# Kernel tuning notes

Hardware: AMD Instinct MI355X
Metric: run time of the kernel (lower is better)

Reference implementation:

```python
import jax, jax.numpy as jnp
import numpy as np

KH = KW = 3
K = KH * KW
PAD = 1


def conv3x3(x, w, b):
    # x: [B,C,H,W], w: [O,C,3,3], b: [O]
    y = jax.lax.conv_general_dilated(x, w, (1, 1), ((PAD, PAD), (PAD, PAD)),
                                     dimension_numbers=('NCHW', 'OIHW', 'NCHW'))
    return y + b[None, :, None, None]


def deform_conv(x, offsets, w, b):
    # torchvision DeformConv2d, stride=1, pad=1, dilation=1, groups=1, offset_groups=1
    # x: [B,C,H,W], offsets: [B,2*K,H,W] ordered (dy,dx) per kernel point, w: [O,C,3,3]
    B, C, H, W = x.shape
    O = w.shape[0]
    off = offsets.reshape(B, K, 2, H, W)
    dy, dx = off[:, :, 0], off[:, :, 1]                      # [B,K,H,W]
    kyy, kxx = jnp.meshgrid(jnp.arange(KH), jnp.arange(KW), indexing='ij')
    ky = kyy.reshape(K).astype(x.dtype)
    kx = kxx.reshape(K).astype(x.dtype)
    py = dy + ky[None, :, None, None] + jnp.arange(H, dtype=x.dtype)[None, None, :, None] - PAD
    px = dx + kx[None, :, None, None] + jnp.arange(W, dtype=x.dtype)[None, None, None, :] - PAD
    y0 = jnp.floor(py)
    x0 = jnp.floor(px)
    wy = (py - y0)[:, None]                                   # [B,1,K,H,W]
    wx = (px - x0)[:, None]
    y0i = y0.astype(jnp.int32)
    x0i = x0.astype(jnp.int32)
    xf = x.reshape(B, C, H * W)

    def gather(yi, xi):
        valid = (yi >= 0) & (yi < H) & (xi >= 0) & (xi < W)   # zero outside
        yc = jnp.clip(yi, 0, H - 1)
        xc = jnp.clip(xi, 0, W - 1)
        idx = (yc * W + xc).reshape(B, 1, K * H * W)
        g = jnp.take_along_axis(xf, idx, axis=2).reshape(B, C, K, H, W)
        return g * valid[:, None].astype(x.dtype)

    v00 = gather(y0i, x0i)
    v01 = gather(y0i, x0i + 1)
    v10 = gather(y0i + 1, x0i)
    v11 = gather(y0i + 1, x0i + 1)
    samp = (v00 * (1 - wy) * (1 - wx) + v01 * (1 - wy) * wx
            + v10 * wy * (1 - wx) + v11 * wy * wx)            # [B,C,K,H,W]
    out = jnp.einsum('bckhw,ock->bohw', samp, w.reshape(O, C, K))
    return out + b[None, :, None, None]


def deform_align(x, y, wo, bo, wd, bd):
    return deform_conv(x, conv3x3(y, wo, bo), wd, bd)


def setup_inputs() -> dict:
    key = jax.random.key(0)
    ks = jax.random.split(key, 16)
    inC, embedC = 64, 96
    B, H, W = 4, 96, 96
    s = 0.02
    d = {
        'x1': jax.random.normal(ks[0], (B, inC, H, W), jnp.float32),
        'y': jax.random.normal(ks[1], (B, inC, H, W), jnp.float32),
        # block 1: offset conv inC->2K, deform conv inC->embedC
        'wo1': jax.random.normal(ks[2], (2 * K, inC, 3, 3), jnp.float32) * s,
        'bo1': jnp.zeros((2 * K,), jnp.float32),
        'wd1': jax.random.normal(ks[3], (embedC, inC, 3, 3), jnp.float32) * s,
        'bd1': jnp.zeros((embedC,), jnp.float32),
        # block 2: embedC->2K, embedC->embedC
        'wo2': jax.random.normal(ks[4], (2 * K, embedC, 3, 3), jnp.float32) * s,
        'bo2': jnp.zeros((2 * K,), jnp.float32),
        'wd2': jax.random.normal(ks[5], (embedC, embedC, 3, 3), jnp.float32) * s,
        'bd2': jnp.zeros((embedC,), jnp.float32),
        # block 3: embedC->2K, embedC->inC
        'wo3': jax.random.normal(ks[6], (2 * K, embedC, 3, 3), jnp.float32) * s,
        'bo3': jnp.zeros((2 * K,), jnp.float32),
        'wd3': jax.random.normal(ks[7], (inC, embedC, 3, 3), jnp.float32) * s,
        'bd3': jnp.zeros((inC,), jnp.float32),
    }
    return d


def reference(x1, y, wo1, bo1, wd1, bd1, wo2, bo2, wd2, bd2, wo3, bo3, wd3, bd3):
    h = deform_align(x1, y, wo1, bo1, wd1, bd1)
    h = deform_align(h, h, wo2, bo2, wd2, bd2)
    h = deform_align(h, h, wo3, bo3, wd3, bd3)
    return h
```

## Files before the change

### kernel.cpp

```cpp
#include <hip/hip_runtime.h>

constexpr int B = 4, H = 96, W = 96, HW = H * W;
constexpr int NPIX = B * HW;
constexpr int KOFF = 18;

typedef _Float16 half8 __attribute__((ext_vector_type(8)));
typedef _Float16 half4 __attribute__((ext_vector_type(4)));
typedef float f32x4 __attribute__((ext_vector_type(4)));

__device__ __forceinline__ int iclamp(int v, int lo, int hi) {
  return v < lo ? lo : (v > hi ? hi : v);
}

struct Corners {
  int i00, i01, i10, i11;
  float w00, w01, w10, w11;
};

__device__ __forceinline__ Corners mk_corners(float py, float qx) {
  float fy = floorf(py), fx = floorf(qx);
  float wy = py - fy, wx = qx - fx;
  int y0 = (int)fy, x0 = (int)fx;
  int y1 = y0 + 1, x1 = x0 + 1;
  bool vy0 = (y0 >= 0) & (y0 < H);
  bool vy1 = (y1 >= 0) & (y1 < H);
  bool vx0 = (x0 >= 0) & (x0 < W);
  bool vx1 = (x1 >= 0) & (x1 < W);
  int r0 = iclamp(y0, 0, H - 1) * W;
  int r1 = iclamp(y1, 0, H - 1) * W;
  int c0 = iclamp(x0, 0, W - 1);
  int c1 = iclamp(x1, 0, W - 1);
  Corners cc;
  cc.i00 = r0 + c0; cc.i01 = r0 + c1; cc.i10 = r1 + c0; cc.i11 = r1 + c1;
  float a = 1.f - wy, bb = 1.f - wx;
  cc.w00 = a * bb * ((vy0 & vx0) ? 1.f : 0.f);
  cc.w01 = a * wx * ((vy0 & vx1) ? 1.f : 0.f);
  cc.w10 = wy * bb * ((vy1 & vx0) ? 1.f : 0.f);
  cc.w11 = wy * wx * ((vy1 & vx1) ? 1.f : 0.f);
  return cc;
}

template <int KS>
__device__ __forceinline__ void load_corners(const _Float16* xb, int ch, const Corners& cc,
                                             half8 r[KS][4]) {
  const _Float16* p00 = xb + (size_t)cc.i00 * (KS * 32) + ch;
  const _Float16* p01 = xb + (size_t)cc.i01 * (KS * 32) + ch;
  const _Float16* p10 = xb + (size_t)cc.i10 * (KS * 32) + ch;
  const _Float16* p11 = xb + (size_t)cc.i11 * (KS * 32) + ch;
#pragma unroll
  for (int ks = 0; ks < KS; ++ks) {
    r[ks][0] = *(const half8*)(p00 + ks * 32);
    r[ks][1] = *(const half8*)(p01 + ks * 32);
    r[ks][2] = *(const half8*)(p10 + ks * 32);
    r[ks][3] = *(const half8*)(p11 + ks * 32);
  }
}

template <int KS>
__device__ __forceinline__ void interp_corners(const Corners& cc, half8 r[KS][4],
                                               half8 a[KS]) {
  _Float16 q00 = (_Float16)cc.w00, q01 = (_Float16)cc.w01;
  _Float16 q10 = (_Float16)cc.w10, q11 = (_Float16)cc.w11;
#pragma unroll
  for (int ks = 0; ks < KS; ++ks)
    a[ks] = r[ks][0] * q00 + r[ks][1] * q01 + r[ks][2] * q10 + r[ks][3] * q11;
}

template <int KS>
__device__ __forceinline__ void load_shift(const _Float16* xb, int ch, int h, int w,
                                           int ky, int kx, half8 a[KS]) {
  int yy = h + ky, xx = w + kx;
  bool v = (yy >= 0) & (yy < H) & (xx >= 0) & (xx < W);
  const _Float16* pv = xb + (size_t)(yy * W + xx) * (KS * 32) + ch;
#pragma unroll
  for (int ks = 0; ks < KS; ++ks) {
    half8 r = {0, 0, 0, 0, 0, 0, 0, 0};
    if (v) r = *(const half8*)(pv + ks * 32);
    a[ks] = r;
  }
}

template <int KS, int NJ>
__device__ __forceinline__ void mfma_tap1(const _Float16* wk, int lane,
                                          half8 a[KS], f32x4 acc[NJ]) {
#pragma unroll
  for (int ks = 0; ks < KS; ++ks)
#pragma unroll
    for (int j = 0; j < NJ; ++j) {
      half8 b = *(const half8*)(wk + ((size_t)(ks * NJ + j) * 64 + lane) * 8);
      acc[j] = __builtin_amdgcn_mfma_f32_16x16x32_f16(a[ks], b, acc[j], 0, 0, 0);
    }
}

struct WAll {
  const float* src[6];
  _Float16* dst[6];
  int C[6], Osrc[6], OPAD[6], base[6];
};

__global__ void wfrag_all_kernel(WAll wa) {
  int bid = blockIdx.x;
  int s = 0;
#pragma unroll
  for (int i = 1; i < 6; ++i) s += (bid >= wa.base[i]) ? 1 : 0;
  int fid = bid - wa.base[s];
  int C = wa.C[s], Osrc = wa.Osrc[s], OPAD = wa.OPAD[s];
  const float* wsrc = wa.src[s];
  _Float16* wf = wa.dst[s];
  int KS = C / 32;
  int NJ = OPAD / 16;
  int lane = threadIdx.x;
  int j = fid % NJ;
  int ks = (fid / NJ) % KS;
  int k = fid / (NJ * KS);
  int o = j * 16 + (lane & 15);
  int c0 = ks * 32 + (lane >> 4) * 8;
  half8 v;
#pragma unroll
  for (int u = 0; u < 8; ++u)
    v[u] = (o < Osrc) ? (_Float16)wsrc[((size_t)o * C + c0 + u) * 9 + k] : (_Float16)0.f;
  *(half8*)(wf + ((size_t)fid * 64 + lane) * 8) = v;
}

__global__ __launch_bounds__(256) void repack2_kernel(const float* __restrict__ in0,
                                                      const float* __restrict__ in1,
                                                      _Float16* __restrict__ o0,
                                                      _Float16* __restrict__ o1) {
  constexpr int C = 64;
  const float* in = blockIdx.y ? in1 : in0;
  _Float16* outh = blockIdx.y ? o1 : o0;
  __shared__ float tile[64 * C];
  int t = threadIdx.x;
  int pix0 = blockIdx.x * 64;
  int b = pix0 / HW;
  int hw0 = pix0 - b * HW;
  int l = t & 63;
  for (int cc = t >> 6; cc < C; cc += 4)
    tile[cc * 64 + l] = in[((size_t)b * C + cc) * HW + hw0 + l];
  __syncthreads();
  int pl = t >> 2;
  int cq = t & 3;
  _Float16* op = outh + (size_t)(pix0 + pl) * C + cq * (C / 4);
#pragma unroll
  for (int c = 0; c < C / 4; c += 4) {
    half4 hv;
#pragma unroll
    for (int u = 0; u < 4; ++u) hv[u] = (_Float16)tile[(cq * (C / 4) + c + u) * 64 + pl];
    *(half4*)(op + c) = hv;
  }
}

template <int C, int O, bool WF32, bool WH>
__global__ __launch_bounds__(64, 2)
void stage_kernel(const _Float16* __restrict__ xoff, const _Float16* __restrict__ xdef,
                  const _Float16* __restrict__ wfo, const float* __restrict__ bo,
                  const _Float16* __restrict__ wfd, const float* __restrict__ bd,
                  float* __restrict__ out, _Float16* __restrict__ outh) {
  constexpr int KS = C / 32;
  constexpr int NJ = O / 16;
  const int lane = threadIdx.x;
  const int row = lane & 15;
  const int kgrp = lane >> 4;
  const int ch = kgrp * 8;
  const int chunk = (blockIdx.x & 7) * (int)(gridDim.x >> 3) + (blockIdx.x >> 3);
  const int px0 = chunk * 16;
  const int b = px0 / HW;
  const int hw0 = px0 - b * HW;
  const int hwm = hw0 + row;
  const int h0 = hwm / W, w0 = hwm - h0 * W;
  const _Float16* xo = xoff + (size_t)b * HW * C;
  const _Float16* xd = xdef + (size_t)b * HW * C;

  __shared__ float lofs[16][KOFF];

  {
    f32x4 aoc[2];
#pragma unroll
    for (int j = 0; j < 2; ++j) {
      int o = j * 16 + row;
      float bv = (o < KOFF) ? bo[o] : 0.f;
      aoc[j] = {bv, bv, bv, bv};
    }
    half8 a[KS];
    load_shift<KS>(xo, ch, h0, w0, -1, -1, a);
#pragma unroll
    for (int k = 0; k < 9; ++k) {
      const _Float16* wk = wfo + (size_t)k * (KS * 2 * 512);
      if (k < 8) {
        int kn = k + 1;
        half8 n[KS];
        load_shift<KS>(xo, ch, h0, w0, kn / 3 - 1, kn % 3 - 1, n);
        mfma_tap1<KS, 2>(wk, lane, a, aoc);
#pragma unroll
        for (int ks = 0; ks < KS; ++ks) a[ks] = n[ks];
      } else {
        mfma_tap1<KS, 2>(wk, lane, a, aoc);
      }
    }
#pragma unroll
    for (int j = 0; j < 2; ++j) {
      int o = j * 16 + row;
      if (o < KOFF) {
#pragma unroll
        for (int r = 0; r < 4; ++r) lofs[kgrp * 4 + r][o] = aoc[j][r];
      }
    }
  }

  float2 of[9];
#pragma unroll
  for (int k = 0; k < 9; ++k) of[k] = {lofs[row][2 * k], lofs[row][2 * k + 1]};
  const float hf = (float)(h0 - 1), wwf = (float)(w0 - 1);

  f32x4 acc[NJ];
#pragma unroll
  for (int j = 0; j < NJ; ++j) {
    float bv = bd[j * 16 + row];
    acc[j] = {bv, bv, bv, bv};
  }
  half8 a[KS];
  {
    Corners cA = mk_corners(of[0].x + hf, of[0].y + wwf);
    half8 r0[KS][4];
    load_corners<KS>(xd, ch, cA, r0);
    interp_corners<KS>(cA, r0, a);
  }
#pragma unroll
  for (int k = 0; k < 9; ++k) {
    const _Float16* wk = wfd + (size_t)k * (KS * NJ * 512);
    if (k < 8) {
      int kn = k + 1;
      float kyf = (float)(kn / 3), kxf = (float)(kn % 3);
      Corners cA = mk_corners(of[kn].x + hf + kyf, of[kn].y + wwf + kxf);
      half8 r0[KS][4];
      load_corners<KS>(xd, ch, cA, r0);
      mfma_tap1<KS, NJ>(wk, lane, a, acc);
      interp_corners<KS>(cA, r0, a);
    } else {
      mfma_tap1<KS, NJ>(wk, lane, a, acc);
    }
  }
#pragma unroll
  for (int j = 0; j < NJ; ++j) {
    int o = j * 16 + row;
#pragma unroll
    for (int r = 0; r < 4; ++r) {
      int p = px0 + kgrp * 4 + r;
      if (WF32) out[((size_t)b * O + o) * HW + (p - b * HW)] = acc[j][r];
      if (WH) outh[(size_t)p * O + o] = (_Float16)acc[j][r];
    }
  }
}

extern "C" void kernel_launch(void* const* d_in, const int* in_sizes, int n_in,
                              void* d_out, int out_size, void* d_ws, size_t ws_size,
                              hipStream_t stream) {
  const float* x1  = (const float*)d_in[0];
  const float* y   = (const float*)d_in[1];
  const float* wo1 = (const float*)d_in[2];
  const float* bo1 = (const float*)d_in[3];
  const float* wd1 = (const float*)d_in[4];
  const float* bd1 = (const float*)d_in[5];
  const float* wo2 = (const float*)d_in[6];
  const float* bo2 = (const float*)d_in[7];
  const float* wd2 = (const float*)d_in[8];
  const float* bd2 = (const float*)d_in[9];
  const float* wo3 = (const float*)d_in[10];
  const float* bo3 = (const float*)d_in[11];
  const float* wd3 = (const float*)d_in[12];
  const float* bd3 = (const float*)d_in[13];
  float* out = (float*)d_out;

  char* p = (char*)d_ws;
  auto alloc = [&](size_t bytes) {
    char* r = p;
    p += (bytes + 255) & ~(size_t)255;
    return r;
  };
  _Float16* Wo1f = (_Float16*)alloc((size_t)9 * 2 * 2 * 512 * 2);
  _Float16* Wo2f = (_Float16*)alloc((size_t)9 * 3 * 2 * 512 * 2);
  _Float16* Wo3f = (_Float16*)alloc((size_t)9 * 3 * 2 * 512 * 2);
  _Float16* W1f  = (_Float16*)alloc((size_t)9 * 2 * 6 * 512 * 2);
  _Float16* W2f  = (_Float16*)alloc((size_t)9 * 3 * 6 * 512 * 2);
  _Float16* W3f  = (_Float16*)alloc((size_t)9 * 3 * 4 * 512 * 2);
  _Float16* x1h = (_Float16*)alloc((size_t)NPIX * 64 * 2);
  _Float16* yh  = (_Float16*)alloc((size_t)NPIX * 64 * 2);
  _Float16* h1h = (_Float16*)alloc((size_t)NPIX * 96 * 2);
  _Float16* h2h = (_Float16*)alloc((size_t)NPIX * 96 * 2);

  WAll wa;
  wa.src[0] = wo1; wa.dst[0] = Wo1f; wa.C[0] = 64; wa.Osrc[0] = 18; wa.OPAD[0] = 32;
  wa.src[1] = wo2; wa.dst[1] = Wo2f; wa.C[1] = 96; wa.Osrc[1] = 18; wa.OPAD[1] = 32;
  wa.src[2] = wo3; wa.dst[2] = Wo3f; wa.C[2] = 96; wa.Osrc[2] = 18; wa.OPAD[2] = 32;
  wa.src[3] = wd1; wa.dst[3] = W1f;  wa.C[3] = 64; wa.Osrc[3] = 96; wa.OPAD[3] = 96;
  wa.src[4] = wd2; wa.dst[4] = W2f;  wa.C[4] = 96; wa.Osrc[4] = 96; wa.OPAD[4] = 96;
  wa.src[5] = wd3; wa.dst[5] = W3f;  wa.C[5] = 96; wa.Osrc[5] = 64; wa.OPAD[5] = 64;
  int base = 0;
  for (int i = 0; i < 6; ++i) {
    wa.base[i] = base;
    base += 9 * (wa.C[i] / 32) * (wa.OPAD[i] / 16);
  }
  hipLaunchKernelGGL(wfrag_all_kernel, dim3(base), dim3(64), 0, stream, wa);
  hipLaunchKernelGGL(repack2_kernel, dim3(NPIX / 64, 2), dim3(256), 0, stream,
                     x1, y, x1h, yh);

  dim3 gs(NPIX / 16);
  dim3 wb(64);

  hipLaunchKernelGGL((stage_kernel<64, 96, false, true>), gs, wb, 0, stream,
                     yh, x1h, Wo1f, bo1, W1f, bd1, (float*)nullptr, h1h);
  hipLaunchKernelGGL((stage_kernel<96, 96, false, true>), gs, wb, 0, stream,
                     h1h, h1h, Wo2f, bo2, W2f, bd2, (float*)nullptr, h2h);
  hipLaunchKernelGGL((stage_kernel<96, 64, true, false>), gs, wb, 0, stream,
                     h2h, h2h, Wo3f, bo3, W3f, bd3, out, (_Float16*)nullptr);
}
```

Measured before the change: 124.1 us.

## Process two 16-pixel tiles per wavefront to reuse weight fragments

Each wavefront now handles 32 pixels as two 16-row MFMA tiles, and every loaded weight fragment feeds two MFMAs instead of one. This halves weight-fragment global/L2 traffic per pixel and the grid size, and gives more independent MFMAs to hide latency. The cost is doubled accumulators and corner registers, which raises VGPR pressure and may cut occupancy under launch_bounds(64,2). It also halves the number of blocks available to fill the GPU. Offsets are now read from LDS directly rather than cached in registers.

```diff
diff --git a/kernel.cpp b/kernel.cpp
--- a/kernel.cpp
+++ b/kernel.cpp
@@ -81,14 +81,16 @@
 }
 
 template <int KS, int NJ>
-__device__ __forceinline__ void mfma_tap1(const _Float16* wk, int lane,
-                                          half8 a[KS], f32x4 acc[NJ]) {
+__device__ __forceinline__ void mfma_dual(const _Float16* wk, int lane,
+                                          half8 a0[KS], half8 a1[KS],
+                                          f32x4 acc0[NJ], f32x4 acc1[NJ]) {
 #pragma unroll
   for (int ks = 0; ks < KS; ++ks)
 #pragma unroll
     for (int j = 0; j < NJ; ++j) {
       half8 b = *(const half8*)(wk + ((size_t)(ks * NJ + j) * 64 + lane) * 8);
-      acc[j] = __builtin_amdgcn_mfma_f32_16x16x32_f16(a[ks], b, acc[j], 0, 0, 0);
+      acc0[j] = __builtin_amdgcn_mfma_f32_16x16x32_f16(a0[ks], b, acc0[j], 0, 0, 0);
+      acc1[j] = __builtin_amdgcn_mfma_f32_16x16x32_f16(a1[ks], b, acc1[j], 0, 0, 0);
     }
 }
 
@@ -163,38 +165,42 @@
   const int kgrp = lane >> 4;
   const int ch = kgrp * 8;
   const int chunk = (blockIdx.x & 7) * (int)(gridDim.x >> 3) + (blockIdx.x >> 3);
-  const int px0 = chunk * 16;
+  const int px0 = chunk * 32;
   const int b = px0 / HW;
   const int hw0 = px0 - b * HW;
-  const int hwm = hw0 + row;
-  const int h0 = hwm / W, w0 = hwm - h0 * W;
+  const int hwm0 = hw0 + row, hwm1 = hw0 + 16 + row;
+  const int h0 = hwm0 / W, w0 = hwm0 - h0 * W;
+  const int h1 = hwm1 / W, w1 = hwm1 - h1 * W;
   const _Float16* xo = xoff + (size_t)b * HW * C;
   const _Float16* xd = xdef + (size_t)b * HW * C;
 
-  __shared__ float lofs[16][KOFF];
+  __shared__ float lofs[32][KOFF];
 
   {
-    f32x4 aoc[2];
+    f32x4 aoc0[2], aoc1[2];
 #pragma unroll
     for (int j = 0; j < 2; ++j) {
       int o = j * 16 + row;
       float bv = (o < KOFF) ? bo[o] : 0.f;
-      aoc[j] = {bv, bv, bv, bv};
-    }
-    half8 a[KS];
-    load_shift<KS>(xo, ch, h0, w0, -1, -1, a);
+      aoc0[j] = {bv, bv, bv, bv};
+      aoc1[j] = {bv, bv, bv, bv};
+    }
+    half8 a0[KS], a1[KS];
+    load_shift<KS>(xo, ch, h0, w0, -1, -1, a0);
+    load_shift<KS>(xo, ch, h1, w1, -1, -1, a1);
 #pragma unroll
     for (int k = 0; k < 9; ++k) {
       const _Float16* wk = wfo + (size_t)k * (KS * 2 * 512);
       if (k < 8) {
         int kn = k + 1;
-        half8 n[KS];
-        load_shift<KS>(xo, ch, h0, w0, kn / 3 - 1, kn % 3 - 1, n);
-        mfma_tap1<KS, 2>(wk, lane, a, aoc);
-#pragma unroll
-        for (int ks = 0; ks < KS; ++ks) a[ks] = n[ks];
+        half8 n0[KS], n1[KS];
+        load_shift<KS>(xo, ch, h0, w0, kn / 3 - 1, kn % 3 - 1, n0);
+        load_shift<KS>(xo, ch, h1, w1, kn / 3 - 1, kn % 3 - 1, n1);
+        mfma_dual<KS, 2>(wk, lane, a0, a1, aoc0, aoc1);
+#pragma unroll
+        for (int ks = 0; ks < KS; ++ks) { a0[ks] = n0[ks]; a1[ks] = n1[ks]; }
       } else {
-        mfma_tap1<KS, 2>(wk, lane, a, aoc);
+        mfma_dual<KS, 2>(wk, lane, a0, a1, aoc0, aoc1);
       }
     }
 #pragma unroll
@@ -202,28 +208,33 @@
       int o = j * 16 + row;
       if (o < KOFF) {
 #pragma unroll
-        for (int r = 0; r < 4; ++r) lofs[kgrp * 4 + r][o] = aoc[j][r];
+        for (int r = 0; r < 4; ++r) {
+          lofs[kgrp * 4 + r][o] = aoc0[j][r];
+          lofs[16 + kgrp * 4 + r][o] = aoc1[j][r];
+        }
       }
     }
   }
 
-  float2 of[9];
-#pragma unroll
-  for (int k = 0; k < 9; ++k) of[k] = {lofs[row][2 * k], lofs[row][2 * k + 1]};
-  const float hf = (float)(h0 - 1), wwf = (float)(w0 - 1);
-
-  f32x4 acc[NJ];
+  const float hf0 = (float)(h0 - 1), wf0_ = (float)(w0 - 1);
+  const float hf1 = (float)(h1 - 1), wf1_ = (float)(w1 - 1);
+
+  f32x4 acc0[NJ], acc1[NJ];
 #pragma unroll
   for (int j = 0; j < NJ; ++j) {
     float bv = bd[j * 16 + row];
-    acc[j] = {bv, bv, bv, bv};
-  }
-  half8 a[KS];
+    acc0[j] = {bv, bv, bv, bv};
+    acc1[j] = {bv, bv, bv, bv};
+  }
+  half8 a0[KS], a1[KS];
   {
-    Corners cA = mk_corners(of[0].x + hf, of[0].y + wwf);
-    half8 r0[KS][4];
+    Corners cA = mk_corners(lofs[row][0] + hf0, lofs[row][1] + wf0_);
+    Corners cB = mk_corners(lofs[16 + row][0] + hf1, lofs[16 + row][1] + wf1_);
+    half8 r0[KS][4], r1[KS][4];
     load_corners<KS>(xd, ch, cA, r0);
-    interp_corners<KS>(cA, r0, a);
+    load_corners<KS>(xd, ch, cB, r1);
+    interp_corners<KS>(cA, r0, a0);
+    interp_corners<KS>(cB, r1, a1);
   }
 #pragma unroll
   for (int k = 0; k < 9; ++k) {
@@ -231,13 +242,18 @@
     if (k < 8) {
       int kn = k + 1;
       float kyf = (float)(kn / 3), kxf = (float)(kn % 3);
-      Corners cA = mk_corners(of[kn].x + hf + kyf, of[kn].y + wwf + kxf);
-      half8 r0[KS][4];
+      Corners cA = mk_corners(lofs[row][2 * kn] + hf0 + kyf,
+                              lofs[row][2 * kn + 1] + wf0_ + kxf);
+      Corners cB = mk_corners(lofs[16 + row][2 * kn] + hf1 + kyf,
+                              lofs[16 + row][2 * kn + 1] + wf1_ + kxf);
+      half8 r0[KS][4], r1[KS][4];
       load_corners<KS>(xd, ch, cA, r0);
-      mfma_tap1<KS, NJ>(wk, lane, a, acc);
-      interp_corners<KS>(cA, r0, a);
+      load_corners<KS>(xd, ch, cB, r1);
+      mfma_dual<KS, NJ>(wk, lane, a0, a1, acc0, acc1);
+      interp_corners<KS>(cA, r0, a0);
+      interp_corners<KS>(cB, r1, a1);
     } else {
-      mfma_tap1<KS, NJ>(wk, lane, a, acc);
+      mfma_dual<KS, NJ>(wk, lane, a0, a1, acc0, acc1);
     }
   }
 #pragma unroll
@@ -245,9 +261,16 @@
     int o = j * 16 + row;
 #pragma unroll
     for (int r = 0; r < 4; ++r) {
-      int p = px0 + kgrp * 4 + r;
-      if (WF32) out[((size_t)b * O + o) * HW + (p - b * HW)] = acc[j][r];
-      if (WH) outh[(size_t)p * O + o] = (_Float16)acc[j][r];
+      int p0 = px0 + kgrp * 4 + r;
+      int p1 = p0 + 16;
+      if (WF32) {
+        out[((size_t)b * O + o) * HW + (p0 - b * HW)] = acc0[j][r];
+        out[((size_t)b * O + o) * HW + (p1 - b * HW)] = acc1[j][r];
+      }
+      if (WH) {
+        outh[(size_t)p0 * O + o] = (_Float16)acc0[j][r];
+        outh[(size_t)p1 * O + o] = (_Float16)acc1[j][r];
+      }
     }
   }
 }
@@ -304,7 +327,7 @@
   hipLaunchKernelGGL(repack2_kernel, dim3(NPIX / 64, 2), dim3(256), 0, stream,
                      x1, y, x1h, yh);
 
-  dim3 gs(NPIX / 16);
+  dim3 gs(NPIX / 32);
   dim3 wb(64);
 
   hipLaunchKernelGGL((stage_kernel<64, 96, false, true>), gs, wb, 0, stream,
```

Measured after the change: 125.6 us. No clear change (+1.2%).

## Stage weight fragments into double-buffered LDS via async global-to-LDS loads

Applied to the files above, without the earlier changes.

Weight fragments for each tap are copied into a double-buffered shared-memory area with global_load_lds, and MFMA B operands are read from LDS instead of global memory. The sampling loop is restructured so the corner gathers for the next tap are issued before the current tap is interpolated and multiplied, with explicit vmcnt waits and scheduling barriers. Shift loads are made unconditional on clamped addresses with a select. Launch bounds drop to one block per SIMD minimum, which raises register headroom but may lower occupancy, and the full vmcnt(0) waits may serialize the prefetch.

```diff
diff --git a/kernel.cpp b/kernel.cpp
--- a/kernel.cpp
+++ b/kernel.cpp
@@ -7,6 +7,7 @@
 typedef _Float16 half8 __attribute__((ext_vector_type(8)));
 typedef _Float16 half4 __attribute__((ext_vector_type(4)));
 typedef float f32x4 __attribute__((ext_vector_type(4)));
+typedef __attribute__((address_space(3))) _Float16 lf16;
 
 __device__ __forceinline__ int iclamp(int v, int lo, int hi) {
   return v < lo ? lo : (v > hi ? hi : v);
@@ -40,6 +41,24 @@
   return cc;
 }
 
+__device__ __forceinline__ void vm_wait0() {
+  asm volatile("s_waitcnt vmcnt(0)" ::: "memory");
+  __builtin_amdgcn_sched_barrier(0);
+}
+
+__device__ __forceinline__ void gld_lds16(const _Float16* g, lf16* l) {
+  __builtin_amdgcn_global_load_lds(
+      (const __attribute__((address_space(1))) void*)g,
+      (__attribute__((address_space(3))) void*)l, 16, 0, 0);
+}
+
+template <int NF>
+__device__ __forceinline__ void stage_frags(const _Float16* wk, lf16* lb, int lane) {
+#pragma unroll
+  for (int f = 0; f < NF; ++f)
+    gld_lds16(wk + (size_t)f * 512 + lane * 8, lb + f * 512);
+}
+
 template <int KS>
 __device__ __forceinline__ void load_corners(const _Float16* xb, int ch, const Corners& cc,
                                              half8 r[KS][4]) {
@@ -71,23 +90,24 @@
                                            int ky, int kx, half8 a[KS]) {
   int yy = h + ky, xx = w + kx;
   bool v = (yy >= 0) & (yy < H) & (xx >= 0) & (xx < W);
-  const _Float16* pv = xb + (size_t)(yy * W + xx) * (KS * 32) + ch;
+  int yc = iclamp(yy, 0, H - 1), xc = iclamp(xx, 0, W - 1);
+  const _Float16* pv = xb + (size_t)(yc * W + xc) * (KS * 32) + ch;
 #pragma unroll
   for (int ks = 0; ks < KS; ++ks) {
-    half8 r = {0, 0, 0, 0, 0, 0, 0, 0};
-    if (v) r = *(const half8*)(pv + ks * 32);
-    a[ks] = r;
+    half8 r = *(const half8*)(pv + ks * 32);
+    half8 z = {0, 0, 0, 0, 0, 0, 0, 0};
+    a[ks] = v ? r : z;
   }
 }
 
 template <int KS, int NJ>
-__device__ __forceinline__ void mfma_tap1(const _Float16* wk, int lane,
-                                          half8 a[KS], f32x4 acc[NJ]) {
+__device__ __forceinline__ void mfma_lds(const _Float16* lb, int lane,
+                                         half8 a[KS], f32x4 acc[NJ]) {
 #pragma unroll
   for (int ks = 0; ks < KS; ++ks)
 #pragma unroll
     for (int j = 0; j < NJ; ++j) {
-      half8 b = *(const half8*)(wk + ((size_t)(ks * NJ + j) * 64 + lane) * 8);
+      half8 b = *(const half8*)(lb + (ks * NJ + j) * 512 + lane * 8);
       acc[j] = __builtin_amdgcn_mfma_f32_16x16x32_f16(a[ks], b, acc[j], 0, 0, 0);
     }
 }
@@ -151,13 +171,18 @@
 }
 
 template <int C, int O, bool WF32, bool WH>
-__global__ __launch_bounds__(64, 2)
+__global__ __launch_bounds__(64, 1)
 void stage_kernel(const _Float16* __restrict__ xoff, const _Float16* __restrict__ xdef,
                   const _Float16* __restrict__ wfo, const float* __restrict__ bo,
                   const _Float16* __restrict__ wfd, const float* __restrict__ bd,
                   float* __restrict__ out, _Float16* __restrict__ outh) {
   constexpr int KS = C / 32;
   constexpr int NJ = O / 16;
+  constexpr int NFD = KS * NJ;
+  constexpr int NFO = KS * 2;
+  __shared__ _Float16 ldsB[2 * NFD * 512];
+  __shared__ float lofs[16][KOFF];
+  lf16* lb3 = (lf16*)ldsB;
   const int lane = threadIdx.x;
   const int row = lane & 15;
   const int kgrp = lane >> 4;
@@ -171,8 +196,6 @@
   const _Float16* xo = xoff + (size_t)b * HW * C;
   const _Float16* xd = xdef + (size_t)b * HW * C;
 
-  __shared__ float lofs[16][KOFF];
-
   {
     f32x4 aoc[2];
 #pragma unroll
@@ -181,20 +204,23 @@
       float bv = (o < KOFF) ? bo[o] : 0.f;
       aoc[j] = {bv, bv, bv, bv};
     }
-    half8 a[KS];
+    half8 a[KS], n[KS];
+    stage_frags<NFO>(wfo, lb3, lane);
     load_shift<KS>(xo, ch, h0, w0, -1, -1, a);
 #pragma unroll
     for (int k = 0; k < 9; ++k) {
-      const _Float16* wk = wfo + (size_t)k * (KS * 2 * 512);
+      vm_wait0();
       if (k < 8) {
         int kn = k + 1;
-        half8 n[KS];
+        stage_frags<NFO>(wfo + (size_t)kn * (NFO * 512),
+                         lb3 + (kn & 1) * NFO * 512, lane);
         load_shift<KS>(xo, ch, h0, w0, kn / 3 - 1, kn % 3 - 1, n);
-        mfma_tap1<KS, 2>(wk, lane, a, aoc);
+        __builtin_amdgcn_sched_barrier(0);
+      }
+      mfma_lds<KS, 2>(ldsB + (k & 1) * NFO * 512, lane, a, aoc);
+      if (k < 8) {
 #pragma unroll
         for (int ks = 0; ks < KS; ++ks) a[ks] = n[ks];
-      } else {
-        mfma_tap1<KS, 2>(wk, lane, a, aoc);
       }
     }
 #pragma unroll
@@ -207,9 +233,6 @@
     }
   }
 
-  float2 of[9];
-#pragma unroll
-  for (int k = 0; k < 9; ++k) of[k] = {lofs[row][2 * k], lofs[row][2 * k + 1]};
   const float hf = (float)(h0 - 1), wwf = (float)(w0 - 1);
 
   f32x4 acc[NJ];
@@ -219,35 +242,41 @@
     acc[j] = {bv, bv, bv, bv};
   }
   half8 a[KS];
-  {
-    Corners cA = mk_corners(of[0].x + hf, of[0].y + wwf);
-    half8 r0[KS][4];
-    load_corners<KS>(xd, ch, cA, r0);
-    interp_corners<KS>(cA, r0, a);
-  }
+  half8 r[KS][4], rn[KS][4];
+  Corners ccur = mk_corners(lofs[row][0] + hf, lofs[row][1] + wwf);
+  stage_frags<NFD>(wfd, lb3 + NFD * 512, lane);
+  load_corners<KS>(xd, ch, ccur, r);
 #pragma unroll
   for (int k = 0; k < 9; ++k) {
-    const _Float16* wk = wfd + (size_t)k * (KS * NJ * 512);
+    vm_wait0();
     if (k < 8) {
       int kn = k + 1;
-      float kyf = (float)(kn / 3), kxf = (float)(kn % 3);
-      Corners cA = mk_corners(of[kn].x + hf + kyf, of[kn].y + wwf + kxf);
-      half8 r0[KS][4];
-      load_corners<KS>(xd, ch, cA, r0);
-      mfma_tap1<KS, NJ>(wk, lane, a, acc);
-      interp_corners<KS>(cA, r0, a);
+      Corners cn = mk_corners(lofs[row][2 * kn] + hf + (float)(kn / 3),
+                              lofs[row][2 * kn + 1] + wwf + (float)(kn % 3));
+      stage_frags<NFD>(wfd + (size_t)kn * (NFD * 512),
+                       lb3 + ((kn + 1) & 1) * NFD * 512, lane);
+      load_corners<KS>(xd, ch, cn, rn);
+      __builtin_amdgcn_sched_barrier(0);
+      interp_corners<KS>(ccur, r, a);
+      mfma_lds<KS, NJ>(ldsB + ((k + 1) & 1) * NFD * 512, lane, a, acc);
+      ccur = cn;
+#pragma unroll
+      for (int ks = 0; ks < KS; ++ks)
+#pragma unroll
+        for (int q = 0; q < 4; ++q) r[ks][q] = rn[ks][q];
     } else {
-      mfma_tap1<KS, NJ>(wk, lane, a, acc);
+      interp_corners<KS>(ccur, r, a);
+      mfma_lds<KS, NJ>(ldsB + ((k + 1) & 1) * NFD * 512, lane, a, acc);
     }
   }
 #pragma unroll
   for (int j = 0; j < NJ; ++j) {
     int o = j * 16 + row;
 #pragma unroll
-    for (int r = 0; r < 4; ++r) {
-      int p = px0 + kgrp * 4 + r;
-      if (WF32) out[((size_t)b * O + o) * HW + (p - b * HW)] = acc[j][r];
-      if (WH) outh[(size_t)p * O + o] = (_Float16)acc[j][r];
+    for (int r2 = 0; r2 < 4; ++r2) {
+      int p = px0 + kgrp * 4 + r2;
+      if (WF32) out[((size_t)b * O + o) * HW + (p - b * HW)] = acc[j][r2];
+      if (WH) outh[(size_t)p * O + o] = (_Float16)acc[j][r2];
     }
   }
 }
```

Result: slower. 135.5 us (+9.2%).
